# Kernel tuning notes

Measured on AMD Instinct MI355X. Metric: run time of the kernel, lower is better.

Reference implementation:

```python
import jax, jax.numpy as jnp
import numpy as np

D_MODEL = 1024
NUM_HEADS = 16
D_K = D_MODEL // NUM_HEADS
B, S = 2, 2048


def setup_inputs() -> dict:
    key = jax.random.key(0)
    ks = jax.random.split(key, 11)
    lim = 1.0 / np.sqrt(D_MODEL)  # torch Linear default init range
    def lin(kw, kb):
        W = jax.random.uniform(kw, (D_MODEL, D_MODEL), jnp.float32, -lim, lim)
        b = jax.random.uniform(kb, (D_MODEL,), jnp.float32, -lim, lim)
        return W, b
    Wq, bq = lin(ks[0], ks[1])
    Wk, bk = lin(ks[2], ks[3])
    Wv, bv = lin(ks[4], ks[5])
    Wo, bo = lin(ks[6], ks[7])
    return {
        "Q": jax.random.normal(ks[8], (B, S, D_MODEL), jnp.float32),
        "K": jax.random.normal(ks[9], (B, S, D_MODEL), jnp.float32),
        "V": jax.random.normal(ks[10], (B, S, D_MODEL), jnp.float32),
        "Wq": Wq, "bq": bq, "Wk": Wk, "bk": bk,
        "Wv": Wv, "bv": bv, "Wo": Wo, "bo": bo,
        "validate": False,
    }


def _split_heads(x):
    b, s, _ = x.shape
    return x.reshape(b, s, NUM_HEADS, D_K).transpose(0, 2, 1, 3)  # [B,H,S,Dk]


def reference(Q, K, V, Wq, bq, Wk, bk, Wv, bv, Wo, bo, validate):
    # Linear projections (torch Linear: x @ W.T + b)
    q = _split_heads(Q @ Wq.T + bq)
    k = _split_heads(K @ Wk.T + bk)
    v = _split_heads(V @ Wv.T + bv)
    scale = 1.0 / jnp.sqrt(jnp.asarray(D_K, q.dtype))
    scores = jnp.einsum("bhqd,bhkd->bhqk", q, k) * scale  # [B,H,S,S]
    attn = jax.nn.softmax(scores, axis=-1)
    out = jnp.einsum("bhqk,bhkd->bhqd", attn, v)  # [B,H,S,Dk]
    out = out.transpose(0, 2, 1, 3).reshape(Q.shape[0], Q.shape[1], D_MODEL)
    return out @ Wo.T + bo
```

## Files before the change

kernel.cpp:

```cpp
#include <hip/hip_runtime.h>


typedef short bf16x8 __attribute__((ext_vector_type(8)));
typedef float f32x4 __attribute__((ext_vector_type(4)));

#define D_MODEL 1024
#define NHEAD 16
#define DK 64
#define BB 2
#define SS 2048
#define MROWS (BB * SS)
#define C1 0.18033688011112042f

__device__ __forceinline__ unsigned short f2bf(float f) {
  unsigned u = __builtin_bit_cast(unsigned, f);
  u += 0x7fffu + ((u >> 16) & 1u);
  return (unsigned short)(u >> 16);
}
__device__ __forceinline__ unsigned pack2(float a, float b) {
  return (unsigned)f2bf(a) | ((unsigned)f2bf(b) << 16);
}
__device__ __forceinline__ unsigned cvtpk(float lo, float hi) {
  unsigned r;
  asm("v_cvt_pk_bf16_f32 %0, %1, %2" : "=v"(r) : "v"(lo), "v"(hi));
  return r;
}

typedef __attribute__((address_space(3))) unsigned int as3u;
typedef const __attribute__((address_space(1))) unsigned int as1u;
__device__ __forceinline__ void gload16(void* lds, const void* g) {
  __builtin_amdgcn_global_load_lds((as1u*)g, (as3u*)lds, 16, 0, 0);
}

struct CvtArgs {
  const float* s[7];
  unsigned short* d[7];
  int n8[7];
};

__global__ __launch_bounds__(256) void convert_bf16(CvtArgs a) {
  const int slot = blockIdx.y;
  const float* __restrict__ s = a.s[slot];
  unsigned short* __restrict__ d = a.d[slot];
  const int n8 = a.n8[slot];
  for (int i = blockIdx.x * 256 + threadIdx.x; i < n8; i += gridDim.x * 256) {
    const size_t off = (size_t)i * 8;
    const float4 v0 = *(const float4*)&s[off];
    const float4 v1 = *(const float4*)&s[off + 4];
    uint4 p;
    p.x = pack2(v0.x, v0.y); p.y = pack2(v0.z, v0.w);
    p.z = pack2(v1.x, v1.y); p.w = pack2(v1.z, v1.w);
    *(uint4*)&d[off] = p;
  }
}

template <int BM, int BN, int MODE>
__device__ __forceinline__ void gemm_core(unsigned short* smem,
                                          const unsigned short* __restrict__ A,
                                          const unsigned short* __restrict__ B,
                                          const float* __restrict__ bias,
                                          float scale, float* __restrict__ Cf,
                                          unsigned short* __restrict__ Cb) {
  unsigned short* As = smem;
  unsigned short* Bs = smem + BM * 64;
  const int tid = threadIdx.x;
  const int lane = tid & 63, w = tid >> 6;
  const int wm = w >> 1, wn = w & 1;
  const int l15 = lane & 15, l4 = lane >> 4;
  const int bm = blockIdx.y, bn = blockIdx.x;
  const int MF = BM / 32, NF = BN / 32;

  f32x4 acc[MF][NF];
#pragma unroll
  for (int m = 0; m < MF; ++m)
#pragma unroll
    for (int n = 0; n < NF; ++n) acc[m][n] = (f32x4){0.f, 0.f, 0.f, 0.f};

  for (int k0 = 0; k0 < D_MODEL; k0 += 64) {
    __syncthreads();
#pragma unroll
    for (int i = 0; i < BM / 32; ++i) {
      const int flat = i * 256 + tid;
      const int row = flat >> 3, g = flat & 7;
      gload16(&As[flat * 8], &A[(size_t)(bm * BM + row) * D_MODEL + k0 + ((g ^ (row & 7)) << 3)]);
    }
#pragma unroll
    for (int i = 0; i < BN / 32; ++i) {
      const int flat = i * 256 + tid;
      const int row = flat >> 3, g = flat & 7;
      gload16(&Bs[flat * 8], &B[(size_t)(bn * BN + row) * D_MODEL + k0 + ((g ^ (row & 7)) << 3)]);
    }
    __syncthreads();
#pragma unroll
    for (int kk = 0; kk < 2; ++kk) {
      bf16x8 af[MF], bf[NF];
#pragma unroll
      for (int m = 0; m < MF; ++m) {
        const int r = wm * (BM / 2) + m * 16 + l15;
        af[m] = *(const bf16x8*)&As[r * 64 + (((kk * 4 + l4) ^ (r & 7)) << 3)];
      }
#pragma unroll
      for (int n = 0; n < NF; ++n) {
        const int r = wn * (BN / 2) + n * 16 + l15;
        bf[n] = *(const bf16x8*)&Bs[r * 64 + (((kk * 4 + l4) ^ (r & 7)) << 3)];
      }
#pragma unroll
      for (int m = 0; m < MF; ++m)
#pragma unroll
        for (int n = 0; n < NF; ++n)
          acc[m][n] = __builtin_amdgcn_mfma_f32_16x16x32_bf16(af[m], bf[n], acc[m][n], 0, 0, 0);
    }
  }

  if (MODE != 2) {
#pragma unroll
    for (int m = 0; m < MF; ++m)
#pragma unroll
      for (int n = 0; n < NF; ++n) {
        const int col = bn * BN + wn * (BN / 2) + n * 16 + l15;
        const float bv = bias[col];
#pragma unroll
        for (int r = 0; r < 4; ++r) {
          const int row = bm * BM + wm * (BM / 2) + m * 16 + l4 * 4 + r;
          const float v = (acc[m][n][r] + bv) * scale;
          if (MODE == 0) Cb[(size_t)row * D_MODEL + col] = f2bf(v);
          else           Cf[(size_t)row * D_MODEL + col] = v;
        }
      }
  } else {
    unsigned short* T = smem;
    __syncthreads();
#pragma unroll
    for (int m = 0; m < MF; ++m)
#pragma unroll
      for (int n = 0; n < NF; ++n) {
        const int cl = wn * (BN / 2) + n * 16 + l15;
        const float bv = bias[bn * BN + cl];
#pragma unroll
        for (int r = 0; r < 4; ++r) {
          const int rl = wm * (BM / 2) + m * 16 + l4 * 4 + r;
          const int byte = cl * (BM * 2) + ((((rl >> 3) ^ (cl & 7))) << 4) + ((rl & 7) << 1);
          *(unsigned short*)((char*)T + byte) = f2bf(acc[m][n][r] + bv);
        }
      }
    __syncthreads();
#pragma unroll
    for (int c = 0; c < BN * BM / 8 / 256; ++c) {
      const int chunk = c * 256 + tid;
      const int cl = chunk >> 3, rl0 = (chunk & 7) * 8;
      const int byte = cl * (BM * 2) + (((rl0 >> 3) ^ (cl & 7)) << 4);
      const uint4 val = *(const uint4*)((const char*)T + byte);
      const int gcol = bn * BN + cl;
      const int bb = (bm * BM) >> 11;
      const int s = ((bm * BM) & 2047) + rl0;
      *(uint4*)&Cb[(size_t)(bb * 1024 + gcol) * SS + s] = val;
    }
  }
}

__global__ __launch_bounds__(256) void gemm_qkv(
    const unsigned short* __restrict__ Xq, const unsigned short* __restrict__ Xk,
    const unsigned short* __restrict__ Xv,
    const unsigned short* __restrict__ Wq, const float* __restrict__ bq,
    const unsigned short* __restrict__ Wk, const float* __restrict__ bk,
    const unsigned short* __restrict__ Wv, const float* __restrict__ bv,
    unsigned short* __restrict__ q, unsigned short* __restrict__ k,
    unsigned short* __restrict__ vT) {
  __shared__ __align__(16) unsigned short smem[(64 + 128) * 64];
  const int z = blockIdx.z;
  if (z == 0) {
    gemm_core<64, 128, 0>(smem, Xq, Wq, bq, C1, nullptr, q);
  } else if (z == 1) {
    gemm_core<64, 128, 0>(smem, Xk, Wk, bk, 1.0f, nullptr, k);
  } else {
    gemm_core<64, 128, 2>(smem, Xv, Wv, bv, 1.0f, nullptr, vT);
  }
}

__global__ __launch_bounds__(256) void gemm_o(const unsigned short* __restrict__ A,
                                              const unsigned short* __restrict__ W,
                                              const float* __restrict__ bi,
                                              float* __restrict__ out) {
  __shared__ __align__(16) unsigned short smem[(64 + 64) * 64];
  gemm_core<64, 64, 1>(smem, A, W, bi, 1.0f, out, nullptr);
}

__global__ __launch_bounds__(256) void attn_kernel(
    const unsigned short* __restrict__ Qp, const unsigned short* __restrict__ Kp,
    const unsigned short* __restrict__ vTp, unsigned short* __restrict__ Op) {
  __shared__ __align__(16) unsigned short Kt[64 * 64];
  __shared__ __align__(16) unsigned short Vt[64 * 64];
  __shared__ __align__(16) unsigned short Pt[4][16 * 64];
  const int tid = threadIdx.x;
  const int lane = tid & 63, w = tid >> 6;
  const int l15 = lane & 15, l4 = lane >> 4;
  const int bh = blockIdx.x;
  const int b = bh >> 4, h = bh & 15;
  const int qb = blockIdx.y;
  const size_t baseQ = (size_t)b * SS * D_MODEL + (size_t)h * DK;
  const size_t baseV = (size_t)(b * 1024 + h * 64) * SS;

  const int qrow = qb * 64 + w * 16 + l15;
  bf16x8 aq[2];
#pragma unroll
  for (int kk = 0; kk < 2; ++kk)
    aq[kk] = *(const bf16x8*)&Qp[baseQ + (size_t)qrow * D_MODEL + kk * 32 + l4 * 8];

  float rm = -1e30f, rs = 0.f;
  f32x4 acc[4];
#pragma unroll
  for (int d = 0; d < 4; ++d) acc[d] = (f32x4){0.f, 0.f, 0.f, 0.f};

  for (int kt = 0; kt < SS / 64; ++kt) {
    __syncthreads();
#pragma unroll
    for (int i = 0; i < 2; ++i) {
      const int flat = (w * 2 + i) * 64 + lane;
      const int row = flat >> 3, g = flat & 7;
      gload16(&Kt[flat * 8], &Kp[baseQ + (size_t)(kt * 64 + row) * D_MODEL + ((g ^ (row & 7)) << 3)]);
    }
#pragma unroll
    for (int i = 0; i < 2; ++i) {
      const int flat = (w * 2 + i) * 64 + lane;
      const int row = flat >> 3, g = flat & 7;
      gload16(&Vt[flat * 8], &vTp[baseV + (size_t)row * SS + kt * 64 + ((g ^ (row & 7)) << 3)]);
    }
    __syncthreads();

    f32x4 st[4];
#pragma unroll
    for (int n = 0; n < 4; ++n) st[n] = (f32x4){0.f, 0.f, 0.f, 0.f};
#pragma unroll
    for (int kk = 0; kk < 2; ++kk) {
      bf16x8 kf[4];
#pragma unroll
      for (int n = 0; n < 4; ++n) {
        const int r = n * 16 + l15;
        kf[n] = *(const bf16x8*)&Kt[r * 64 + (((kk * 4 + l4) ^ (r & 7)) << 3)];
      }
#pragma unroll
      for (int n = 0; n < 4; ++n)
        st[n] = __builtin_amdgcn_mfma_f32_16x16x32_bf16(kf[n], aq[kk], st[n], 0, 0, 0);
    }

    float mx = st[0][0];
#pragma unroll
    for (int n = 0; n < 4; ++n)
#pragma unroll
      for (int r = 0; r < 4; ++r) mx = fmaxf(mx, st[n][r]);
    mx = fmaxf(mx, __shfl_xor(mx, 16));
    mx = fmaxf(mx, __shfl_xor(mx, 32));
    if (__any(mx > rm)) {
      const float nm = fmaxf(rm, mx);
      const float alpha = exp2f(rm - nm);
      rm = nm;
      rs *= alpha;
#pragma unroll
      for (int r = 0; r < 4; ++r) {
        const float ar = __shfl(alpha, l4 * 4 + r);
#pragma unroll
        for (int d = 0; d < 4; ++d) acc[d][r] *= ar;
      }
    }
    float ps = 0.f;
#pragma unroll
    for (int n = 0; n < 4; ++n)
#pragma unroll
      for (int r = 0; r < 4; ++r) {
        const float p = exp2f(st[n][r] - rm);
        st[n][r] = p;
        ps += p;
      }
    ps += __shfl_xor(ps, 16);
    ps += __shfl_xor(ps, 32);
    rs += ps;

#pragma unroll
    for (int n = 0; n < 4; ++n)
#pragma unroll
      for (int c = 0; c < 2; ++c) {
        const int col = n * 16 + l4 * 4 + 2 * c;
        const int sw = (((col >> 3) ^ (l15 & 7)) << 3) + (col & 7);
        *(unsigned*)&Pt[w][l15 * 64 + sw] = cvtpk(st[n][2 * c], st[n][2 * c + 1]);
      }

#pragma unroll
    for (int kk = 0; kk < 2; ++kk) {
      const bf16x8 ap = *(const bf16x8*)&Pt[w][l15 * 64 + (((kk * 4 + l4) ^ (l15 & 7)) << 3)];
      bf16x8 vf[4];
#pragma unroll
      for (int d = 0; d < 4; ++d) {
        const int r = d * 16 + l15;
        vf[d] = *(const bf16x8*)&Vt[r * 64 + (((kk * 4 + l4) ^ (r & 7)) << 3)];
      }
#pragma unroll
      for (int d = 0; d < 4; ++d)
        acc[d] = __builtin_amdgcn_mfma_f32_16x16x32_bf16(ap, vf[d], acc[d], 0, 0, 0);
    }
  }

  float rsb[4];
#pragma unroll
  for (int r = 0; r < 4; ++r) rsb[r] = __shfl(rs, l4 * 4 + r);
#pragma unroll
  for (int d = 0; d < 4; ++d)
#pragma unroll
    for (int r = 0; r < 4; ++r) {
      const int orow = qb * 64 + w * 16 + l4 * 4 + r;
      Op[baseQ + (size_t)orow * D_MODEL + d * 16 + l15] = f2bf(acc[d][r] / rsb[r]);
    }
}

extern "C" void kernel_launch(void* const* d_in, const int* in_sizes, int n_in,
                              void* d_out, int out_size, void* d_ws, size_t ws_size,
                              hipStream_t stream) {
  const float* Qin = (const float*)d_in[0];
  const float* Kin = (const float*)d_in[1];
  const float* Vin = (const float*)d_in[2];
  const float* Wq = (const float*)d_in[3];
  const float* bq = (const float*)d_in[4];
  const float* Wk = (const float*)d_in[5];
  const float* bk = (const float*)d_in[6];
  const float* Wv = (const float*)d_in[7];
  const float* bv = (const float*)d_in[8];
  const float* Wo = (const float*)d_in[9];
  const float* bo = (const float*)d_in[10];
  float* out = (float*)d_out;

  const size_t NX = (size_t)MROWS * D_MODEL;
  const size_t NW = (size_t)D_MODEL * D_MODEL;
  unsigned short* ws = (unsigned short*)d_ws;
  unsigned short* q  = ws;
  unsigned short* k  = ws + NX;
  unsigned short* vT = ws + 2 * NX;
  unsigned short* Xq = ws + 3 * NX;
  unsigned short* Xk = ws + 4 * NX;
  unsigned short* Xv = ws + 5 * NX;
  unsigned short* wq = ws + 6 * NX;
  unsigned short* wk = wq + NW;
  unsigned short* wv = wk + NW;
  unsigned short* wo = wv + NW;
  unsigned short* ao = Xq;

  CvtArgs ca;
  ca.s[0] = Qin; ca.d[0] = Xq; ca.n8[0] = (int)(NX / 8);
  ca.s[1] = Kin; ca.d[1] = Xk; ca.n8[1] = (int)(NX / 8);
  ca.s[2] = Vin; ca.d[2] = Xv; ca.n8[2] = (int)(NX / 8);
  ca.s[3] = Wq;  ca.d[3] = wq; ca.n8[3] = (int)(NW / 8);
  ca.s[4] = Wk;  ca.d[4] = wk; ca.n8[4] = (int)(NW / 8);
  ca.s[5] = Wv;  ca.d[5] = wv; ca.n8[5] = (int)(NW / 8);
  ca.s[6] = Wo;  ca.d[6] = wo; ca.n8[6] = (int)(NW / 8);
  convert_bf16<<<dim3(1024, 7), 256, 0, stream>>>(ca);

  gemm_qkv<<<dim3(D_MODEL / 128, MROWS / 64, 3), 256, 0, stream>>>(
      Xq, Xk, Xv, wq, bq, wk, bk, wv, bv, q, k, vT);
  attn_kernel<<<dim3(BB * NHEAD, SS / 64), 256, 0, stream>>>(q, k, vT, ao);
  gemm_o<<<dim3(D_MODEL / 64, MROWS / 64), 256, 0, stream>>>(ao, wo, bo, out);
}
```

Measured before the change: 252.4 us.

## Double-buffer GEMM and attention LDS, lazy rescale, MFMA row sums, wider gemm_o tiles

The GEMM core and the attention kernel now double-buffer their LDS tiles, so the next tile's global-to-LDS loads are issued before computing on the current one, with one barrier per iteration instead of two. The attention softmax uses v_max3 for the row max and only rescales when the max grows by more than 8 (in log2 units). Row sums are computed by an extra MFMA against a ones vector instead of shuffle reductions, and the final normalisation multiplies by a reciprocal. gemm_o moves to 64x128 tiles, and occupancy hints are added to the launch bounds. The larger LDS footprint may lower occupancy, and the lazy rescale lets probabilities exceed 1 before normalisation, which adds some bf16 rounding risk.

Result: faster. 237.2 us (-6.0%).

```diff
diff --git a/kernel.cpp b/kernel.cpp
--- a/kernel.cpp
+++ b/kernel.cpp
@@ -24,6 +24,11 @@
   unsigned r;
   asm("v_cvt_pk_bf16_f32 %0, %1, %2" : "=v"(r) : "v"(lo), "v"(hi));
   return r;
+}
+__device__ __forceinline__ float max3f(float a, float b, float c) {
+  float d;
+  asm("v_max3_f32 %0, %1, %2, %3" : "=v"(d) : "v"(a), "v"(b), "v"(c));
+  return d;
 }
 
 typedef __attribute__((address_space(3))) unsigned int as3u;
@@ -61,8 +66,7 @@
                                           const float* __restrict__ bias,
                                           float scale, float* __restrict__ Cf,
                                           unsigned short* __restrict__ Cb) {
-  unsigned short* As = smem;
-  unsigned short* Bs = smem + BM * 64;
+  const int LDSZ = (BM + BN) * 64;
   const int tid = threadIdx.x;
   const int lane = tid & 63, w = tid >> 6;
   const int wm = w >> 1, wn = w & 1;
@@ -70,27 +74,36 @@
   const int bm = blockIdx.y, bn = blockIdx.x;
   const int MF = BM / 32, NF = BN / 32;
 
-  f32x4 acc[MF][NF];
-#pragma unroll
-  for (int m = 0; m < MF; ++m)
-#pragma unroll
-    for (int n = 0; n < NF; ++n) acc[m][n] = (f32x4){0.f, 0.f, 0.f, 0.f};
-
-  for (int k0 = 0; k0 < D_MODEL; k0 += 64) {
-    __syncthreads();
+  auto stage = [&](unsigned short* dst, int k0) {
+    unsigned short* Asb = dst;
+    unsigned short* Bsb = dst + BM * 64;
 #pragma unroll
     for (int i = 0; i < BM / 32; ++i) {
       const int flat = i * 256 + tid;
       const int row = flat >> 3, g = flat & 7;
-      gload16(&As[flat * 8], &A[(size_t)(bm * BM + row) * D_MODEL + k0 + ((g ^ (row & 7)) << 3)]);
+      gload16(&Asb[flat * 8], &A[(size_t)(bm * BM + row) * D_MODEL + k0 + ((g ^ (row & 7)) << 3)]);
     }
 #pragma unroll
     for (int i = 0; i < BN / 32; ++i) {
       const int flat = i * 256 + tid;
       const int row = flat >> 3, g = flat & 7;
-      gload16(&Bs[flat * 8], &B[(size_t)(bn * BN + row) * D_MODEL + k0 + ((g ^ (row & 7)) << 3)]);
-    }
-    __syncthreads();
+      gload16(&Bsb[flat * 8], &B[(size_t)(bn * BN + row) * D_MODEL + k0 + ((g ^ (row & 7)) << 3)]);
+    }
+  };
+
+  f32x4 acc[MF][NF];
+#pragma unroll
+  for (int m = 0; m < MF; ++m)
+#pragma unroll
+    for (int n = 0; n < NF; ++n) acc[m][n] = (f32x4){0.f, 0.f, 0.f, 0.f};
+
+  stage(smem, 0);
+  __syncthreads();
+  int cur = 0;
+  for (int k0 = 0; k0 < D_MODEL; k0 += 64) {
+    if (k0 + 64 < D_MODEL) stage(smem + (cur ^ 1) * LDSZ, k0 + 64);
+    unsigned short* As = smem + cur * LDSZ;
+    unsigned short* Bs = As + BM * 64;
 #pragma unroll
     for (int kk = 0; kk < 2; ++kk) {
       bf16x8 af[MF], bf[NF];
@@ -110,6 +123,8 @@
         for (int n = 0; n < NF; ++n)
           acc[m][n] = __builtin_amdgcn_mfma_f32_16x16x32_bf16(af[m], bf[n], acc[m][n], 0, 0, 0);
     }
+    __syncthreads();
+    cur ^= 1;
   }
 
   if (MODE != 2) {
@@ -129,7 +144,6 @@
       }
   } else {
     unsigned short* T = smem;
-    __syncthreads();
 #pragma unroll
     for (int m = 0; m < MF; ++m)
 #pragma unroll
@@ -158,7 +172,7 @@
   }
 }
 
-__global__ __launch_bounds__(256) void gemm_qkv(
+__global__ __launch_bounds__(256, 3) void gemm_qkv(
     const unsigned short* __restrict__ Xq, const unsigned short* __restrict__ Xk,
     const unsigned short* __restrict__ Xv,
     const unsigned short* __restrict__ Wq, const float* __restrict__ bq,
@@ -166,7 +180,7 @@
     const unsigned short* __restrict__ Wv, const float* __restrict__ bv,
     unsigned short* __restrict__ q, unsigned short* __restrict__ k,
     unsigned short* __restrict__ vT) {
-  __shared__ __align__(16) unsigned short smem[(64 + 128) * 64];
+  __shared__ __align__(16) unsigned short smem[2 * (64 + 128) * 64];
   const int z = blockIdx.z;
   if (z == 0) {
     gemm_core<64, 128, 0>(smem, Xq, Wq, bq, C1, nullptr, q);
@@ -177,19 +191,19 @@
   }
 }
 
-__global__ __launch_bounds__(256) void gemm_o(const unsigned short* __restrict__ A,
-                                              const unsigned short* __restrict__ W,
-                                              const float* __restrict__ bi,
-                                              float* __restrict__ out) {
-  __shared__ __align__(16) unsigned short smem[(64 + 64) * 64];
-  gemm_core<64, 64, 1>(smem, A, W, bi, 1.0f, out, nullptr);
-}
-
-__global__ __launch_bounds__(256) void attn_kernel(
+__global__ __launch_bounds__(256, 3) void gemm_o(const unsigned short* __restrict__ A,
+                                                 const unsigned short* __restrict__ W,
+                                                 const float* __restrict__ bi,
+                                                 float* __restrict__ out) {
+  __shared__ __align__(16) unsigned short smem[2 * (64 + 128) * 64];
+  gemm_core<64, 128, 1>(smem, A, W, bi, 1.0f, out, nullptr);
+}
+
+__global__ __launch_bounds__(256, 4) void attn_kernel(
     const unsigned short* __restrict__ Qp, const unsigned short* __restrict__ Kp,
     const unsigned short* __restrict__ vTp, unsigned short* __restrict__ Op) {
-  __shared__ __align__(16) unsigned short Kt[64 * 64];
-  __shared__ __align__(16) unsigned short Vt[64 * 64];
+  __shared__ __align__(16) unsigned short Kt[2][64 * 64];
+  __shared__ __align__(16) unsigned short Vt[2][64 * 64];
   __shared__ __align__(16) unsigned short Pt[4][16 * 64];
   const int tid = threadIdx.x;
   const int lane = tid & 63, w = tid >> 6;
@@ -206,26 +220,35 @@
   for (int kk = 0; kk < 2; ++kk)
     aq[kk] = *(const bf16x8*)&Qp[baseQ + (size_t)qrow * D_MODEL + kk * 32 + l4 * 8];
 
-  float rm = -1e30f, rs = 0.f;
-  f32x4 acc[4];
-#pragma unroll
-  for (int d = 0; d < 4; ++d) acc[d] = (f32x4){0.f, 0.f, 0.f, 0.f};
-
-  for (int kt = 0; kt < SS / 64; ++kt) {
-    __syncthreads();
+  const bf16x8 vone = {0x3F80, 0x3F80, 0x3F80, 0x3F80, 0x3F80, 0x3F80, 0x3F80, 0x3F80};
+
+  float rm = -1e30f;
+  f32x4 acc[5];
+#pragma unroll
+  for (int d = 0; d < 5; ++d) acc[d] = (f32x4){0.f, 0.f, 0.f, 0.f};
+
+  auto stage = [&](int buf, int kt) {
 #pragma unroll
     for (int i = 0; i < 2; ++i) {
       const int flat = (w * 2 + i) * 64 + lane;
       const int row = flat >> 3, g = flat & 7;
-      gload16(&Kt[flat * 8], &Kp[baseQ + (size_t)(kt * 64 + row) * D_MODEL + ((g ^ (row & 7)) << 3)]);
+      gload16(&Kt[buf][flat * 8],
+              &Kp[baseQ + (size_t)(kt * 64 + row) * D_MODEL + ((g ^ (row & 7)) << 3)]);
     }
 #pragma unroll
     for (int i = 0; i < 2; ++i) {
       const int flat = (w * 2 + i) * 64 + lane;
       const int row = flat >> 3, g = flat & 7;
-      gload16(&Vt[flat * 8], &vTp[baseV + (size_t)row * SS + kt * 64 + ((g ^ (row & 7)) << 3)]);
-    }
-    __syncthreads();
+      gload16(&Vt[buf][flat * 8],
+              &vTp[baseV + (size_t)row * SS + kt * 64 + ((g ^ (row & 7)) << 3)]);
+    }
+  };
+
+  stage(0, 0);
+  __syncthreads();
+  int cur = 0;
+  for (int kt = 0; kt < SS / 64; ++kt) {
+    if (kt + 1 < SS / 64) stage(cur ^ 1, kt + 1);
 
     f32x4 st[4];
 #pragma unroll
@@ -236,44 +259,36 @@
 #pragma unroll
       for (int n = 0; n < 4; ++n) {
         const int r = n * 16 + l15;
-        kf[n] = *(const bf16x8*)&Kt[r * 64 + (((kk * 4 + l4) ^ (r & 7)) << 3)];
+        kf[n] = *(const bf16x8*)&Kt[cur][r * 64 + (((kk * 4 + l4) ^ (r & 7)) << 3)];
       }
 #pragma unroll
       for (int n = 0; n < 4; ++n)
         st[n] = __builtin_amdgcn_mfma_f32_16x16x32_bf16(kf[n], aq[kk], st[n], 0, 0, 0);
     }
 
-    float mx = st[0][0];
-#pragma unroll
-    for (int n = 0; n < 4; ++n)
-#pragma unroll
-      for (int r = 0; r < 4; ++r) mx = fmaxf(mx, st[n][r]);
+    const float a0 = max3f(st[0][0], st[0][1], st[0][2]);
+    const float a1 = max3f(st[0][3], st[1][0], st[1][1]);
+    const float a2 = max3f(st[1][2], st[1][3], st[2][0]);
+    const float a3 = max3f(st[2][1], st[2][2], st[2][3]);
+    const float a4 = max3f(st[3][0], st[3][1], st[3][2]);
+    float mx = fmaxf(max3f(a0, a1, a2), max3f(a3, a4, st[3][3]));
     mx = fmaxf(mx, __shfl_xor(mx, 16));
     mx = fmaxf(mx, __shfl_xor(mx, 32));
-    if (__any(mx > rm)) {
+    if (__any(mx > rm + 8.f)) {
       const float nm = fmaxf(rm, mx);
       const float alpha = exp2f(rm - nm);
       rm = nm;
-      rs *= alpha;
 #pragma unroll
       for (int r = 0; r < 4; ++r) {
         const float ar = __shfl(alpha, l4 * 4 + r);
 #pragma unroll
-        for (int d = 0; d < 4; ++d) acc[d][r] *= ar;
-      }
-    }
-    float ps = 0.f;
+        for (int d = 0; d < 5; ++d) acc[d][r] *= ar;
+      }
+    }
 #pragma unroll
     for (int n = 0; n < 4; ++n)
 #pragma unroll
-      for (int r = 0; r < 4; ++r) {
-        const float p = exp2f(st[n][r] - rm);
-        st[n][r] = p;
-        ps += p;
-      }
-    ps += __shfl_xor(ps, 16);
-    ps += __shfl_xor(ps, 32);
-    rs += ps;
+      for (int r = 0; r < 4; ++r) st[n][r] = exp2f(st[n][r] - rm);
 
 #pragma unroll
     for (int n = 0; n < 4; ++n)
@@ -291,23 +306,27 @@
 #pragma unroll
       for (int d = 0; d < 4; ++d) {
         const int r = d * 16 + l15;
-        vf[d] = *(const bf16x8*)&Vt[r * 64 + (((kk * 4 + l4) ^ (r & 7)) << 3)];
+        vf[d] = *(const bf16x8*)&Vt[cur][r * 64 + (((kk * 4 + l4) ^ (r & 7)) << 3)];
       }
 #pragma unroll
       for (int d = 0; d < 4; ++d)
         acc[d] = __builtin_amdgcn_mfma_f32_16x16x32_bf16(ap, vf[d], acc[d], 0, 0, 0);
-    }
-  }
-
-  float rsb[4];
-#pragma unroll
-  for (int r = 0; r < 4; ++r) rsb[r] = __shfl(rs, l4 * 4 + r);
+      acc[4] = __builtin_amdgcn_mfma_f32_16x16x32_bf16(ap, vone, acc[4], 0, 0, 0);
+    }
+
+    __syncthreads();
+    cur ^= 1;
+  }
+
+  float inv[4];
+#pragma unroll
+  for (int r = 0; r < 4; ++r) inv[r] = 1.0f / acc[4][r];
 #pragma unroll
   for (int d = 0; d < 4; ++d)
 #pragma unroll
     for (int r = 0; r < 4; ++r) {
       const int orow = qb * 64 + w * 16 + l4 * 4 + r;
-      Op[baseQ + (size_t)orow * D_MODEL + d * 16 + l15] = f2bf(acc[d][r] / rsb[r]);
+      Op[baseQ + (size_t)orow * D_MODEL + d * 16 + l15] = f2bf(acc[d][r] * inv[r]);
     }
 }
 
@@ -355,5 +374,5 @@
   gemm_qkv<<<dim3(D_MODEL / 128, MROWS / 64, 3), 256, 0, stream>>>(
       Xq, Xk, Xv, wq, bq, wk, bk, wv, bv, q, k, vT);
   attn_kernel<<<dim3(BB * NHEAD, SS / 64), 256, 0, stream>>>(q, k, vT, ao);
-  gemm_o<<<dim3(D_MODEL / 64, MROWS / 64), 256, 0, stream>>>(ao, wo, bo, out);
-}
+  gemm_o<<<dim3(D_MODEL / 128, MROWS / 64), 256, 0, stream>>>(ao, wo, bo, out);
+}
```
